# Kernel tuning notes

Measured on AMD Instinct MI355X. Metric: run time of the kernel, lower is better.

Reference implementation:

```python
import jax, jax.numpy as jnp
import numpy as np

N = 50000      # total nodes
E = 400000     # edges (before self-loops)
F_IN = 75      # atom features
H = 4          # GAT heads (layers 1,2)
C = 128        # hidden_channels
G = 512        # graphs in batch
EPS_BN = 1e-5


def setup_inputs() -> dict:
    key = jax.random.key(0)
    ks = jax.random.split(key, 32)
    inp = {}
    inp["x"] = jax.random.normal(ks[0], (N, F_IN), jnp.float32)
    inp["edge_index"] = jax.random.randint(ks[1], (2, E), 0, N, dtype=jnp.int32)
    inp["batch"] = jnp.sort(jax.random.randint(ks[2], (N,), 0, G, dtype=jnp.int32))
    # (in_dim, heads, out_per_head, concat)
    dims = [(F_IN, H, C, True), (H * C, H, C, True), (H * C, 1, C, False)]
    i = 3
    for li, (din, h, c, concat) in enumerate(dims, 1):
        dout = h * c if concat else c
        s = 1.0 / np.sqrt(din)
        inp[f"W{li}"] = jax.random.normal(ks[i], (din, h * c), jnp.float32) * s
        inp[f"as{li}"] = jax.random.normal(ks[i + 1], (h, c), jnp.float32) * 0.1
        inp[f"ad{li}"] = jax.random.normal(ks[i + 2], (h, c), jnp.float32) * 0.1
        inp[f"b{li}"] = jnp.zeros((dout,), jnp.float32)
        inp[f"g{li}"] = jnp.ones((dout,), jnp.float32)
        inp[f"bt{li}"] = jnp.zeros((dout,), jnp.float32)
        inp[f"rm{li}"] = jax.random.normal(ks[i + 3], (dout,), jnp.float32) * 0.05
        inp[f"rv{li}"] = jnp.ones((dout,), jnp.float32)
        i += 4
    return inp


def gat_layer(x, src, dst, W, a_src, a_dst, b, heads, c_out, concat):
    # x: [N, Fin] -> h: [N, H, C]
    n = x.shape[0]
    h = (x @ W).reshape(n, heads, c_out)
    # per-node attention logits [N, H]
    al_s = jnp.sum(h * a_src[None], axis=-1)
    al_d = jnp.sum(h * a_dst[None], axis=-1)
    # per-edge logits + leaky relu (PyG GATConv, slope 0.2)
    e = jax.nn.leaky_relu(al_s[src] + al_d[dst], negative_slope=0.2)  # [E, H]
    # segment softmax over destination nodes
    emax = jax.ops.segment_max(e, dst, num_segments=n)
    p = jnp.exp(e - emax[dst])
    denom = jax.ops.segment_sum(p, dst, num_segments=n)
    alpha = p / (denom[dst] + 1e-16)
    # weighted message aggregation
    msg = h[src] * alpha[:, :, None]            # [E, H, C]
    out = jax.ops.segment_sum(msg, dst, num_segments=n)  # [N, H, C]
    out = out.reshape(n, heads * c_out) if concat else out.mean(axis=1)
    return out + b


def bn_eval(x, g, bt, rm, rv):
    return (x - rm) * g * jax.lax.rsqrt(rv + EPS_BN) + bt


def reference(x, edge_index, batch,
              W1, as1, ad1, b1, g1, bt1, rm1, rv1,
              W2, as2, ad2, b2, g2, bt2, rm2, rv2,
              W3, as3, ad3, b3, g3, bt3, rm3, rv3):
    n = x.shape[0]
    ar = jnp.arange(n, dtype=edge_index.dtype)
    # GATConv adds self-loops by default
    src = jnp.concatenate([edge_index[0], ar])
    dst = jnp.concatenate([edge_index[1], ar])

    h = gat_layer(x, src, dst, W1, as1, ad1, b1, H, C, True)
    h = jax.nn.relu(bn_eval(h, g1, bt1, rm1, rv1))   # dropout off (eval)
    h = gat_layer(h, src, dst, W2, as2, ad2, b2, H, C, True)
    h = jax.nn.relu(bn_eval(h, g2, bt2, rm2, rv2))
    h = gat_layer(h, src, dst, W3, as3, ad3, b3, 1, C, False)
    h = bn_eval(h, g3, bt3, rm3, rv3)

    # global mean + max pool over graphs
    ones = jnp.ones((n,), h.dtype)
    cnt = jnp.maximum(jax.ops.segment_sum(ones, batch, num_segments=G), 1.0)
    gmean = jax.ops.segment_sum(h, batch, num_segments=G) / cnt[:, None]
    gmax = jax.ops.segment_max(h, batch, num_segments=G)
    gmax = jnp.where(jnp.isfinite(gmax), gmax, 0.0)  # guard empty graphs
    return jnp.concatenate([gmean, gmax], axis=1)    # [G, 2*C]
```

## Files before the change

### kernel.cpp

```cpp
#include <hip/hip_runtime.h>

typedef unsigned short u16;
typedef unsigned int u32;
typedef __attribute__((ext_vector_type(8))) short s16x8;
typedef __attribute__((ext_vector_type(4))) float f32x4;

__device__ __forceinline__ float bf2f(u32 u) {
    return __uint_as_float(u << 16);
}
__device__ __forceinline__ u16 f2bf(float f) {
    u32 x = __float_as_uint(f);
    u32 r = (x + 0x7fffu + ((x >> 16) & 1u)) >> 16;
    return (u16)r;
}

__device__ __forceinline__ void gload16(const u16* g, u16* l) {
    __builtin_amdgcn_global_load_lds(
        (const __attribute__((address_space(1))) unsigned int*)g,
        (__attribute__((address_space(3))) unsigned int*)l,
        16, 0, 0);
}

__device__ __forceinline__ float lk60(float e) {
    e = (e > 0.f) ? e : 0.2f * e;
    return fminf(e, 60.f);
}

__global__ __launch_bounds__(256) void cvtx_k(
    const float* __restrict__ x, u16* __restrict__ xb, int N, int Mp)
{
    const int i = blockIdx.x * 256 + threadIdx.x;
    if (i >= Mp * 96) return;
    const int r = i / 96, c = i - r * 96;
    float v = (r < N && c < 75) ? x[(size_t)r * 75 + c] : 0.f;
    xb[i] = f2bf(v);
}

__global__ __launch_bounds__(256) void cvtw_k(
    const float* __restrict__ W, u16* __restrict__ Wt, int K, int Kp, int Ncol)
{
    const int i = blockIdx.x * 256 + threadIdx.x;
    if (i >= Ncol * Kp) return;
    const int n = i / Kp, k = i - n * Kp;
    Wt[i] = f2bf(k < K ? W[(size_t)k * Ncol + n] : 0.f);
}

__global__ __launch_bounds__(256) void mgemm_k(
    const u16* __restrict__ A, const u16* __restrict__ Bt, u16* __restrict__ C,
    const float* __restrict__ avs, const float* __restrict__ avd,
    float* __restrict__ als, float* __restrict__ ald,
    int M, int K, int Ncol, int H, int NXB)
{
    __shared__ u16 Al[2][128 * 32];
    __shared__ u16 Bl[2][128 * 32];
    const int t = threadIdx.x;
    const int lane = t & 63;
    const int wid = t >> 6;
    const int wr = wid >> 1, wc = wid & 1;
    const int rr = lane & 15, q = lane >> 4;

    const int dd = blockIdx.x;
    const int xcd = dd & 7, ii = dd >> 3;
    const int gpx = (int)(gridDim.x >> 3) / NXB;
    const int yb = xcd * gpx + ((NXB == 4) ? (ii >> 2) : ii);
    const int head = (NXB == 4) ? (ii & 3) : 0;
    const int m0 = yb * 128, n0 = head * 128;

    f32x4 acc[4][4];
#pragma unroll
    for (int m = 0; m < 4; ++m)
#pragma unroll
        for (int n = 0; n < 4; ++n) acc[m][n] = (f32x4){0.f, 0.f, 0.f, 0.f};

    auto stage = [&](int b, int k0) {
#pragma unroll
        for (int i2 = 0; i2 < 2; ++i2) {
            const int si = i2 * 256 + t;
            const int r = si >> 2, s = si & 3;
            const int g = s ^ ((r >> 1) & 3);
            gload16(A  + (size_t)(m0 + r) * K + k0 + g * 8, &Al[b][si * 8]);
            gload16(Bt + (size_t)(n0 + r) * K + k0 + g * 8, &Bl[b][si * 8]);
        }
    };

    const int nk = K >> 5;
    stage(0, 0);
    __syncthreads();
    int buf = 0;
    for (int kt = 0; kt < nk; ++kt) {
        if (kt + 1 < nk) stage(buf ^ 1, (kt + 1) << 5);
        s16x8 af[4], bfr[4];
#pragma unroll
        for (int m = 0; m < 4; ++m) {
            const int r = wr * 64 + m * 16 + rr;
            af[m] = *reinterpret_cast<const s16x8*>(&Al[buf][r * 32 + ((q ^ ((r >> 1) & 3)) << 3)]);
        }
#pragma unroll
        for (int n = 0; n < 4; ++n) {
            const int r = wc * 64 + n * 16 + rr;
            bfr[n] = *reinterpret_cast<const s16x8*>(&Bl[buf][r * 32 + ((q ^ ((r >> 1) & 3)) << 3)]);
        }
#pragma unroll
        for (int m = 0; m < 4; ++m)
#pragma unroll
            for (int n = 0; n < 4; ++n)
                acc[m][n] = __builtin_amdgcn_mfma_f32_16x16x32_bf16(af[m], bfr[n], acc[m][n], 0, 0, 0);
        __syncthreads();
        buf ^= 1;
    }

#pragma unroll
    for (int m = 0; m < 4; ++m) {
        const int row_b = m0 + wr * 64 + m * 16 + q * 4;
#pragma unroll
        for (int j = 0; j < 4; ++j) {
            const int row = row_b + j;
            if (row < M) {
#pragma unroll
                for (int n = 0; n < 4; ++n) {
                    const int col = n0 + wc * 64 + n * 16 + rr;
                    C[(size_t)row * Ncol + col] = f2bf(acc[m][n][j]);
                }
            }
        }
    }

    float asv[4], adv[4];
#pragma unroll
    for (int n = 0; n < 4; ++n) {
        const int c = wc * 64 + n * 16 + rr;
        asv[n] = avs[head * 128 + c];
        adv[n] = avd[head * 128 + c];
    }
    float* lps = (float*)&Al[0][0];
    float* lpd = lps + 256;
#pragma unroll
    for (int m = 0; m < 4; ++m)
#pragma unroll
        for (int j = 0; j < 4; ++j) {
            float ps = 0.f, pd = 0.f;
#pragma unroll
            for (int n = 0; n < 4; ++n) {
                ps += acc[m][n][j] * asv[n];
                pd += acc[m][n][j] * adv[n];
            }
#pragma unroll
            for (int off = 1; off < 16; off <<= 1) {
                ps += __shfl_xor(ps, off, 64);
                pd += __shfl_xor(pd, off, 64);
            }
            if (rr == 0) {
                const int r = wr * 64 + m * 16 + q * 4 + j;
                lps[wc * 128 + r] = ps;
                lpd[wc * 128 + r] = pd;
            }
        }
    __syncthreads();
    if (t < 128) {
        const int row = m0 + t;
        if (row < M) {
            als[(size_t)row * H + head] = lps[t] + lps[128 + t];
            ald[(size_t)row * H + head] = lpd[t] + lpd[128 + t];
        }
    }
}

__global__ void count_k(const int* __restrict__ edst, int* __restrict__ cnt, int E_, int N_)
{
    const int i = blockIdx.x * 256 + threadIdx.x;
    if (i >= E_ + N_) return;
    const int d = (i < E_) ? edst[i] : (i - E_);
    atomicAdd(&cnt[d], 1);
}

#define SCAN_B 256
__global__ void scan1_k(const int* __restrict__ cnt, int* __restrict__ part,
                        int* __restrict__ bsum, int n)
{
    __shared__ int sm[SCAN_B];
    const int idx = blockIdx.x * SCAN_B + threadIdx.x;
    int v = (idx < n) ? cnt[idx] : 0;
    sm[threadIdx.x] = v;
    __syncthreads();
    for (int off = 1; off < SCAN_B; off <<= 1) {
        int t2 = (threadIdx.x >= off) ? sm[threadIdx.x - off] : 0;
        __syncthreads();
        sm[threadIdx.x] += t2;
        __syncthreads();
    }
    if (idx < n) part[idx] = sm[threadIdx.x];
    if (threadIdx.x == SCAN_B - 1) bsum[blockIdx.x] = sm[threadIdx.x];
}

__global__ void scan2_k(int* __restrict__ bsum, int nb)
{
    __shared__ int sm[SCAN_B];
    const int t = threadIdx.x;
    int v = (t < nb) ? bsum[t] : 0;
    sm[t] = v;
    __syncthreads();
    for (int off = 1; off < SCAN_B; off <<= 1) {
        int t2 = (t >= off) ? sm[t - off] : 0;
        __syncthreads();
        sm[t] += t2;
        __syncthreads();
    }
    if (t < nb) bsum[t] = sm[t] - v;
}

__global__ void scan3_k(const int* __restrict__ part, const int* __restrict__ boff,
                        int* __restrict__ offs, int n)
{
    const int idx = blockIdx.x * SCAN_B + threadIdx.x;
    if (idx < n) offs[idx + 1] = part[idx] + boff[idx / SCAN_B];
    if (idx == 0) offs[0] = 0;
}

__global__ void scatter_k(const int* __restrict__ esrc, const int* __restrict__ edst,
                          const int* __restrict__ offs, int* __restrict__ fill,
                          int* __restrict__ csr, int E_, int N_)
{
    const int i = blockIdx.x * 256 + threadIdx.x;
    if (i >= E_ + N_) return;
    int s, d;
    if (i < E_) { s = esrc[i]; d = edst[i]; } else { s = d = i - E_; }
    const int pos = offs[d] + atomicAdd(&fill[d], 1);
    csr[pos] = s;
}

template<int CH, int C, int SPLIT, bool RELU>
__global__ __launch_bounds__(256) void agg_k(
    const u16* __restrict__ hsrc, const int* __restrict__ offs,
    const int* __restrict__ csr, const float* __restrict__ als,
    const float* __restrict__ ald, const float* __restrict__ bias,
    const float* __restrict__ gam, const float* __restrict__ bet,
    const float* __restrict__ rmean, const float* __restrict__ rvar,
    u16* __restrict__ outp, int N)
{
    constexpr int HH = CH / C;
    constexpr int PW = CH / SPLIT;
    constexpr int Kc = PW / 64;
    constexpr int HPW = (PW + C - 1) / C;
    const int lane = threadIdx.x & 63;
    const int wid = threadIdx.x >> 6;
    const int dst = blockIdx.x * (4 / SPLIT) + (SPLIT == 1 ? wid : (wid >> 1));
    if (dst >= N) return;
    const int half = (SPLIT == 1) ? 0 : (wid & (SPLIT - 1));
    const int ch0 = half * PW + lane * Kc;
    const int hd = ch0 / C;
    const int h0 = half * HPW;

    float adv[HPW];
#pragma unroll
    for (int h = 0; h < HPW; ++h) adv[h] = ald[(size_t)dst * HH + h0 + h];

    const int rs = offs[dst], re = offs[dst + 1];

    float smv[HPW];
#pragma unroll
    for (int h = 0; h < HPW; ++h) smv[h] = 0.f;
    for (int s = rs + lane; s < re; s += 64) {
        const int sn = csr[s];
        if constexpr (HPW == 2) {
            const float2 av = *reinterpret_cast<const float2*>(&als[(size_t)sn * HH + h0]);
            smv[0] += __expf(lk60(av.x + adv[0]));
            smv[1] += __expf(lk60(av.y + adv[1]));
        } else {
            smv[0] += __expf(lk60(als[(size_t)sn * HH + h0] + adv[0]));
        }
    }
#pragma unroll
    for (int h = 0; h < HPW; ++h)
#pragma unroll
        for (int off = 32; off; off >>= 1) smv[h] += __shfl_xor(smv[h], off, 64);
    const float invh = 1.f / (smv[hd - h0] + 1e-16f);
    const float advh = adv[hd - h0];

    float acc[Kc] = {};
    int s = rs;
    for (; s + 4 <= re; s += 4) {
        int sn[4];
#pragma unroll
        for (int u = 0; u < 4; ++u) sn[u] = csr[s + u];
        if constexpr (Kc == 4) {
            uint2 r[4];
#pragma unroll
            for (int u = 0; u < 4; ++u)
                r[u] = *reinterpret_cast<const uint2*>(hsrc + (size_t)sn[u] * CH + ch0);
            float aa[4];
#pragma unroll
            for (int u = 0; u < 4; ++u)
                aa[u] = __expf(lk60(als[(size_t)sn[u] * HH + hd] + advh)) * invh;
#pragma unroll
            for (int u = 0; u < 4; ++u) {
                acc[0] += aa[u] * bf2f(r[u].x & 0xffffu);
                acc[1] += aa[u] * bf2f(r[u].x >> 16);
                acc[2] += aa[u] * bf2f(r[u].y & 0xffffu);
                acc[3] += aa[u] * bf2f(r[u].y >> 16);
            }
        } else {
            u32 r[4];
#pragma unroll
            for (int u = 0; u < 4; ++u)
                r[u] = *reinterpret_cast<const u32*>(hsrc + (size_t)sn[u] * CH + ch0);
            float aa[4];
#pragma unroll
            for (int u = 0; u < 4; ++u)
                aa[u] = __expf(lk60(als[(size_t)sn[u] * HH + hd] + advh)) * invh;
#pragma unroll
            for (int u = 0; u < 4; ++u) {
                acc[0] += aa[u] * bf2f(r[u] & 0xffffu);
                acc[1] += aa[u] * bf2f(r[u] >> 16);
            }
        }
    }
    for (; s < re; ++s) {
        const int sn = csr[s];
        const float a = __expf(lk60(als[(size_t)sn * HH + hd] + advh)) * invh;
        const u16* hp = hsrc + (size_t)sn * CH + ch0;
        if constexpr (Kc == 4) {
            const uint2 r = *reinterpret_cast<const uint2*>(hp);
            acc[0] += a * bf2f(r.x & 0xffffu);
            acc[1] += a * bf2f(r.x >> 16);
            acc[2] += a * bf2f(r.y & 0xffffu);
            acc[3] += a * bf2f(r.y >> 16);
        } else {
            const u32 r = *reinterpret_cast<const u32*>(hp);
            acc[0] += a * bf2f(r & 0xffffu);
            acc[1] += a * bf2f(r >> 16);
        }
    }

    u16 ob[Kc];
#pragma unroll
    for (int j = 0; j < Kc; ++j) {
        const int ch = ch0 + j;
        const float scale = gam[ch] * rsqrtf(rvar[ch] + 1e-5f);
        float val = (acc[j] + bias[ch] - rmean[ch]) * scale + bet[ch];
        if (RELU) val = fmaxf(val, 0.f);
        ob[j] = f2bf(val);
    }
    u16* op = outp + (size_t)dst * CH + ch0;
    if constexpr (Kc == 4) {
        uint2 w;
        w.x = (u32)ob[0] | ((u32)ob[1] << 16);
        w.y = (u32)ob[2] | ((u32)ob[3] << 16);
        *reinterpret_cast<uint2*>(op) = w;
    } else {
        *reinterpret_cast<u32*>(op) = (u32)ob[0] | ((u32)ob[1] << 16);
    }
}

__global__ __launch_bounds__(128) void pool_k(
    const u16* __restrict__ h3, const int* __restrict__ batch,
    float* __restrict__ out, int N)
{
    const int g = blockIdx.x;
    const int t = threadIdx.x;
    int lo = 0, hi = N;
    while (lo < hi) { int mid = (lo + hi) >> 1; if (batch[mid] < g) lo = mid + 1; else hi = mid; }
    const int s0 = lo;
    lo = 0; hi = N;
    while (lo < hi) { int mid = (lo + hi) >> 1; if (batch[mid] < g + 1) lo = mid + 1; else hi = mid; }
    const int s1 = lo;
    float sum = 0.f, mx = -1e30f;
    for (int n = s0; n < s1; ++n) {
        const float v = bf2f((u32)h3[(size_t)n * 128 + t]);
        sum += v;
        mx = fmaxf(mx, v);
    }
    const int cnt = s1 - s0;
    out[(size_t)g * 256 + t]       = cnt ? sum / (float)cnt : 0.f;
    out[(size_t)g * 256 + 128 + t] = cnt ? mx : 0.f;
}

extern "C" void kernel_launch(void* const* d_in, const int* in_sizes, int n_in,
                              void* d_out, int out_size, void* d_ws, size_t ws_size,
                              hipStream_t stream)
{
    const float* x   = (const float*)d_in[0];
    const int* ei    = (const int*)d_in[1];
    const int* batch = (const int*)d_in[2];
    const float* W1  = (const float*)d_in[3];
    const float* as1 = (const float*)d_in[4];
    const float* ad1 = (const float*)d_in[5];
    const float* b1  = (const float*)d_in[6];
    const float* g1  = (const float*)d_in[7];
    const float* bt1 = (const float*)d_in[8];
    const float* rm1 = (const float*)d_in[9];
    const float* rv1 = (const float*)d_in[10];
    const float* W2  = (const float*)d_in[11];
    const float* as2 = (const float*)d_in[12];
    const float* ad2 = (const float*)d_in[13];
    const float* b2  = (const float*)d_in[14];
    const float* g2  = (const float*)d_in[15];
    const float* bt2 = (const float*)d_in[16];
    const float* rm2 = (const float*)d_in[17];
    const float* rv2 = (const float*)d_in[18];
    const float* W3  = (const float*)d_in[19];
    const float* as3 = (const float*)d_in[20];
    const float* ad3 = (const float*)d_in[21];
    const float* b3  = (const float*)d_in[22];
    const float* g3  = (const float*)d_in[23];
    const float* bt3 = (const float*)d_in[24];
    const float* rm3 = (const float*)d_in[25];
    const float* rv3 = (const float*)d_in[26];

    const int Nn = in_sizes[2];
    const int Ee = in_sizes[1] / 2;
    const int ET = Ee + Nn;
    const int Gg = out_size / 256;
    const int Mp = 392 * 128;

    char* ws = (char*)d_ws;
    size_t o = 0;
    auto alc = [&](size_t bytes) { size_t r = o; o = (o + bytes + 255) & ~(size_t)255; return r; };
    u16*  hA   = (u16*)(ws + alc((size_t)Mp * 512 * 2));
    u16*  hB   = (u16*)(ws + alc((size_t)Mp * 512 * 2));
    u16*  xb   = (u16*)(ws + alc((size_t)Mp * 96 * 2));
    u16*  Wt1  = (u16*)(ws + alc((size_t)512 * 96 * 2));
    u16*  Wt2  = (u16*)(ws + alc((size_t)512 * 512 * 2));
    u16*  Wt3  = (u16*)(ws + alc((size_t)128 * 512 * 2));
    float* als = (float*)(ws + alc((size_t)Nn * 4 * 4));
    float* ald = (float*)(ws + alc((size_t)Nn * 4 * 4));
    int*  cnt  = (int*)(ws + alc((size_t)2 * Nn * 4));
    int*  fill = cnt + Nn;
    int*  offs = (int*)(ws + alc((size_t)(Nn + 1) * 4));
    int*  part = (int*)(ws + alc((size_t)Nn * 4));
    int*  bsum = (int*)(ws + alc((size_t)SCAN_B * 4));
    int*  csr  = (int*)(ws + alc((size_t)ET * 4));
    (void)ws_size; (void)n_in;

    hipMemsetAsync(cnt, 0, (size_t)2 * Nn * 4, stream);
    const int ETB = (ET + 255) / 256;
    count_k<<<ETB, 256, 0, stream>>>(ei + Ee, cnt, Ee, Nn);
    const int nb = (Nn + SCAN_B - 1) / SCAN_B;
    scan1_k<<<nb, SCAN_B, 0, stream>>>(cnt, part, bsum, Nn);
    scan2_k<<<1, SCAN_B, 0, stream>>>(bsum, nb);
    scan3_k<<<nb, SCAN_B, 0, stream>>>(part, bsum, offs, Nn);
    scatter_k<<<ETB, 256, 0, stream>>>(ei, ei + Ee, offs, fill, csr, Ee, Nn);

    cvtx_k<<<(Mp * 96 + 255) / 256, 256, 0, stream>>>(x, xb, Nn, Mp);
    cvtw_k<<<(512 * 96 + 255) / 256, 256, 0, stream>>>(W1, Wt1, 75, 96, 512);
    cvtw_k<<<(512 * 512 + 255) / 256, 256, 0, stream>>>(W2, Wt2, 512, 512, 512);
    cvtw_k<<<(128 * 512 + 255) / 256, 256, 0, stream>>>(W3, Wt3, 512, 512, 128);

    const int nwb2 = (Nn + 1) / 2;
    const int nwb4 = (Nn + 3) / 4;
    const int nwg4 = 392 * 4;
    const int nwg1 = 392;

    mgemm_k<<<nwg4, 256, 0, stream>>>(xb, Wt1, hA, as1, ad1, als, ald, Nn, 96, 512, 4, 4);
    agg_k<512, 128, 2, true><<<nwb2, 256, 0, stream>>>(hA, offs, csr, als, ald,
                                                       b1, g1, bt1, rm1, rv1, hB, Nn);
    mgemm_k<<<nwg4, 256, 0, stream>>>(hB, Wt2, hA, as2, ad2, als, ald, Nn, 512, 512, 4, 4);
    agg_k<512, 128, 2, true><<<nwb2, 256, 0, stream>>>(hA, offs, csr, als, ald,
                                                       b2, g2, bt2, rm2, rv2, hB, Nn);
    mgemm_k<<<nwg1, 256, 0, stream>>>(hB, Wt3, hA, as3, ad3, als, ald, Nn, 512, 128, 1, 1);
    agg_k<128, 128, 1, false><<<nwb4, 256, 0, stream>>>(hA, offs, csr, als, ald,
                                                        b3, g3, bt3, rm3, rv3, hB, Nn);
    pool_k<<<Gg, 128, 0, stream>>>(hB, batch, (float*)d_out, Nn);
}
```

Before: 414.5 us.

## Slice GAT aggregation into 64-channel slices with 16-lane groups per destination

Replaces the wavefront-per-destination aggregation with a kernel where each 16-lane group handles one destination node for a 64-channel slice, and blocks are split across channel slices. Each wavefront now serves four destinations at once, so short neighbor lists no longer leave most lanes idle and there are more independent gathers in flight. In exchange, the softmax denominator is recomputed for every slice, which adds redundant exp work and CSR/logit reads. Lanes in a wavefront also now diverge when their destinations have different degrees.

```diff
diff --git a/kernel.cpp b/kernel.cpp
--- a/kernel.cpp
+++ b/kernel.cpp
@@ -228,126 +228,86 @@
     csr[pos] = s;
 }
 
-template<int CH, int C, int SPLIT, bool RELU>
-__global__ __launch_bounds__(256) void agg_k(
+template<int CH, bool RELU>
+__global__ __launch_bounds__(256) void sagg_k(
     const u16* __restrict__ hsrc, const int* __restrict__ offs,
     const int* __restrict__ csr, const float* __restrict__ als,
     const float* __restrict__ ald, const float* __restrict__ bias,
     const float* __restrict__ gam, const float* __restrict__ bet,
     const float* __restrict__ rmean, const float* __restrict__ rvar,
-    u16* __restrict__ outp, int N)
-{
-    constexpr int HH = CH / C;
-    constexpr int PW = CH / SPLIT;
-    constexpr int Kc = PW / 64;
-    constexpr int HPW = (PW + C - 1) / C;
+    u16* __restrict__ outp, int N, int nbs)
+{
+    constexpr int S  = CH / 64;
+    constexpr int HH = CH / 128;
+    const int b = blockIdx.x;
+    int slice, gi;
+    if constexpr (S == 8) { slice = b & 7; gi = b >> 3; }
+    else { slice = (b >= nbs) ? 1 : 0; gi = b - slice * nbs; }
     const int lane = threadIdx.x & 63;
-    const int wid = threadIdx.x >> 6;
-    const int dst = blockIdx.x * (4 / SPLIT) + (SPLIT == 1 ? wid : (wid >> 1));
-    if (dst >= N) return;
-    const int half = (SPLIT == 1) ? 0 : (wid & (SPLIT - 1));
-    const int ch0 = half * PW + lane * Kc;
-    const int hd = ch0 / C;
-    const int h0 = half * HPW;
-
-    float adv[HPW];
-#pragma unroll
-    for (int h = 0; h < HPW; ++h) adv[h] = ald[(size_t)dst * HH + h0 + h];
-
-    const int rs = offs[dst], re = offs[dst + 1];
-
-    float smv[HPW];
-#pragma unroll
-    for (int h = 0; h < HPW; ++h) smv[h] = 0.f;
-    for (int s = rs + lane; s < re; s += 64) {
-        const int sn = csr[s];
-        if constexpr (HPW == 2) {
-            const float2 av = *reinterpret_cast<const float2*>(&als[(size_t)sn * HH + h0]);
-            smv[0] += __expf(lk60(av.x + adv[0]));
-            smv[1] += __expf(lk60(av.y + adv[1]));
-        } else {
-            smv[0] += __expf(lk60(als[(size_t)sn * HH + h0] + adv[0]));
-        }
-    }
-#pragma unroll
-    for (int h = 0; h < HPW; ++h)
-#pragma unroll
-        for (int off = 32; off; off >>= 1) smv[h] += __shfl_xor(smv[h], off, 64);
-    const float invh = 1.f / (smv[hd - h0] + 1e-16f);
-    const float advh = adv[hd - h0];
-
-    float acc[Kc] = {};
+    const int w = threadIdx.x >> 6;
+    const int g = lane >> 4, l = lane & 15;
+    const int dst = gi * 16 + w * 4 + g;
+    const bool valid = dst < N;
+    const int ch0 = slice * 64 + l * 4;
+    const int hd = ch0 >> 7;
+    const int rs = valid ? offs[dst] : 0;
+    const int re = valid ? offs[dst + 1] : 0;
+    const float advh = valid ? ald[(size_t)dst * HH + hd] : 0.f;
+
+    float sm = 0.f;
+    for (int s = rs + l; s < re; s += 16)
+        sm += __expf(lk60(als[(size_t)csr[s] * HH + hd] + advh));
+#pragma unroll
+    for (int off = 8; off; off >>= 1) sm += __shfl_xor(sm, off, 64);
+    const float inv = 1.f / (sm + 1e-16f);
+
+    float a0 = 0.f, a1 = 0.f, a2 = 0.f, a3 = 0.f;
     int s = rs;
     for (; s + 4 <= re; s += 4) {
         int sn[4];
 #pragma unroll
         for (int u = 0; u < 4; ++u) sn[u] = csr[s + u];
-        if constexpr (Kc == 4) {
-            uint2 r[4];
-#pragma unroll
-            for (int u = 0; u < 4; ++u)
-                r[u] = *reinterpret_cast<const uint2*>(hsrc + (size_t)sn[u] * CH + ch0);
-            float aa[4];
-#pragma unroll
-            for (int u = 0; u < 4; ++u)
-                aa[u] = __expf(lk60(als[(size_t)sn[u] * HH + hd] + advh)) * invh;
-#pragma unroll
-            for (int u = 0; u < 4; ++u) {
-                acc[0] += aa[u] * bf2f(r[u].x & 0xffffu);
-                acc[1] += aa[u] * bf2f(r[u].x >> 16);
-                acc[2] += aa[u] * bf2f(r[u].y & 0xffffu);
-                acc[3] += aa[u] * bf2f(r[u].y >> 16);
-            }
-        } else {
-            u32 r[4];
-#pragma unroll
-            for (int u = 0; u < 4; ++u)
-                r[u] = *reinterpret_cast<const u32*>(hsrc + (size_t)sn[u] * CH + ch0);
-            float aa[4];
-#pragma unroll
-            for (int u = 0; u < 4; ++u)
-                aa[u] = __expf(lk60(als[(size_t)sn[u] * HH + hd] + advh)) * invh;
-#pragma unroll
-            for (int u = 0; u < 4; ++u) {
-                acc[0] += aa[u] * bf2f(r[u] & 0xffffu);
-                acc[1] += aa[u] * bf2f(r[u] >> 16);
-            }
+        uint2 r[4];
+#pragma unroll
+        for (int u = 0; u < 4; ++u)
+            r[u] = *reinterpret_cast<const uint2*>(hsrc + (size_t)sn[u] * CH + ch0);
+        float aa[4];
+#pragma unroll
+        for (int u = 0; u < 4; ++u)
+            aa[u] = __expf(lk60(als[(size_t)sn[u] * HH + hd] + advh)) * inv;
+#pragma unroll
+        for (int u = 0; u < 4; ++u) {
+            a0 += aa[u] * bf2f(r[u].x & 0xffffu);
+            a1 += aa[u] * bf2f(r[u].x >> 16);
+            a2 += aa[u] * bf2f(r[u].y & 0xffffu);
+            a3 += aa[u] * bf2f(r[u].y >> 16);
         }
     }
     for (; s < re; ++s) {
         const int sn = csr[s];
-        const float a = __expf(lk60(als[(size_t)sn * HH + hd] + advh)) * invh;
-        const u16* hp = hsrc + (size_t)sn * CH + ch0;
-        if constexpr (Kc == 4) {
-            const uint2 r = *reinterpret_cast<const uint2*>(hp);
-            acc[0] += a * bf2f(r.x & 0xffffu);
-            acc[1] += a * bf2f(r.x >> 16);
-            acc[2] += a * bf2f(r.y & 0xffffu);
-            acc[3] += a * bf2f(r.y >> 16);
-        } else {
-            const u32 r = *reinterpret_cast<const u32*>(hp);
-            acc[0] += a * bf2f(r & 0xffffu);
-            acc[1] += a * bf2f(r >> 16);
-        }
-    }
-
-    u16 ob[Kc];
-#pragma unroll
-    for (int j = 0; j < Kc; ++j) {
-        const int ch = ch0 + j;
-        const float scale = gam[ch] * rsqrtf(rvar[ch] + 1e-5f);
-        float val = (acc[j] + bias[ch] - rmean[ch]) * scale + bet[ch];
-        if (RELU) val = fmaxf(val, 0.f);
-        ob[j] = f2bf(val);
-    }
-    u16* op = outp + (size_t)dst * CH + ch0;
-    if constexpr (Kc == 4) {
-        uint2 w;
-        w.x = (u32)ob[0] | ((u32)ob[1] << 16);
-        w.y = (u32)ob[2] | ((u32)ob[3] << 16);
-        *reinterpret_cast<uint2*>(op) = w;
-    } else {
-        *reinterpret_cast<u32*>(op) = (u32)ob[0] | ((u32)ob[1] << 16);
+        const uint2 r = *reinterpret_cast<const uint2*>(hsrc + (size_t)sn * CH + ch0);
+        const float a = __expf(lk60(als[(size_t)sn * HH + hd] + advh)) * inv;
+        a0 += a * bf2f(r.x & 0xffffu);
+        a1 += a * bf2f(r.x >> 16);
+        a2 += a * bf2f(r.y & 0xffffu);
+        a3 += a * bf2f(r.y >> 16);
+    }
+
+    if (valid) {
+        float av[4] = {a0, a1, a2, a3};
+        u16 ob[4];
+#pragma unroll
+        for (int j = 0; j < 4; ++j) {
+            const int ch = ch0 + j;
+            const float scale = gam[ch] * rsqrtf(rvar[ch] + 1e-5f);
+            float val = (av[j] + bias[ch] - rmean[ch]) * scale + bet[ch];
+            if (RELU) val = fmaxf(val, 0.f);
+            ob[j] = f2bf(val);
+        }
+        uint2 wv;
+        wv.x = (u32)ob[0] | ((u32)ob[1] << 16);
+        wv.y = (u32)ob[2] | ((u32)ob[3] << 16);
+        *reinterpret_cast<uint2*>(outp + (size_t)dst * CH + ch0) = wv;
     }
 }
 
@@ -445,19 +405,18 @@
     cvtw_k<<<(512 * 512 + 255) / 256, 256, 0, stream>>>(W2, Wt2, 512, 512, 512);
     cvtw_k<<<(128 * 512 + 255) / 256, 256, 0, stream>>>(W3, Wt3, 512, 512, 128);
 
-    const int nwb2 = (Nn + 1) / 2;
-    const int nwb4 = (Nn + 3) / 4;
+    const int nbs = (Nn + 15) / 16;
     const int nwg4 = 392 * 4;
     const int nwg1 = 392;
 
     mgemm_k<<<nwg4, 256, 0, stream>>>(xb, Wt1, hA, as1, ad1, als, ald, Nn, 96, 512, 4, 4);
-    agg_k<512, 128, 2, true><<<nwb2, 256, 0, stream>>>(hA, offs, csr, als, ald,
-                                                       b1, g1, bt1, rm1, rv1, hB, Nn);
+    sagg_k<512, true><<<8 * nbs, 256, 0, stream>>>(hA, offs, csr, als, ald,
+                                                   b1, g1, bt1, rm1, rv1, hB, Nn, nbs);
     mgemm_k<<<nwg4, 256, 0, stream>>>(hB, Wt2, hA, as2, ad2, als, ald, Nn, 512, 512, 4, 4);
-    agg_k<512, 128, 2, true><<<nwb2, 256, 0, stream>>>(hA, offs, csr, als, ald,
-                                                       b2, g2, bt2, rm2, rv2, hB, Nn);
+    sagg_k<512, true><<<8 * nbs, 256, 0, stream>>>(hA, offs, csr, als, ald,
+                                                   b2, g2, bt2, rm2, rv2, hB, Nn, nbs);
     mgemm_k<<<nwg1, 256, 0, stream>>>(hB, Wt3, hA, as3, ad3, als, ald, Nn, 512, 128, 1, 1);
-    agg_k<128, 128, 1, false><<<nwb4, 256, 0, stream>>>(hA, offs, csr, als, ald,
-                                                        b3, g3, bt3, rm3, rv3, hB, Nn);
+    sagg_k<128, false><<<2 * nbs, 256, 0, stream>>>(hA, offs, csr, als, ald,
+                                                    b3, g3, bt3, rm3, rv3, hB, Nn, nbs);
     pool_k<<<Gg, 128, 0, stream>>>(hB, batch, (float*)d_out, Nn);
 }
```

Result: slower. 438.2 us (+5.7%).
